# Kernel optimization log

Hardware: AMD Instinct MI355X
Metric: run time of the kernel (lower is better)

## Reference

```python
import jax, jax.numpy as jnp
import numpy as np


def setup_inputs() -> dict:
    key = jax.random.key(0)
    k1, k2, k3 = jax.random.split(key, 3)
    CAP, IN_F, OUT_F = 262144, 512, 512
    query = jax.random.normal(k1, (IN_F,), dtype=jnp.float32)
    keys = jax.random.normal(k2, (CAP, IN_F), dtype=jnp.float32)
    values = jax.random.normal(k3, (CAP, OUT_F), dtype=jnp.float32)
    return {"query": query, "keys": keys, "values": values}


def reference(query, keys, values):
    # L1 distance of query to every key: [capacity]
    attention = -jnp.sum(jnp.abs(keys - query), axis=1)
    # softmax over the capacity dimension
    attention = jax.nn.softmax(attention, axis=0)
    # attention-weighted sum of values: [out_features]
    out = jnp.matmul(attention, values)
    out = jax.nn.sigmoid(out)
    return out
```

## Files before the change

### kernel.cpp

```cpp
#include <hip/hip_runtime.h>
#include <math.h>

typedef float f32x4 __attribute__((ext_vector_type(4)));

constexpr int CAP = 262144;
constexpr int NF  = 512;

constexpr int G1  = 2048;
constexpr int RPB = CAP / G1;
constexpr int GR  = 64;
constexpr int RPR = G1 / GR;

constexpr float CUT = 25.0f;

__global__ __launch_bounds__(256) void k_logits(
    const float* __restrict__ q, const float* __restrict__ keys,
    float* __restrict__ logits, float* __restrict__ pm, float* __restrict__ ps)
{
    const int tid  = threadIdx.x;
    const int lane = tid & 63;
    const int wv   = tid >> 6;
    const int w    = blockIdx.x * 4 + wv;
    const int row0 = w * 32;

    const f32x4 q0 = *reinterpret_cast<const f32x4*>(q + lane * 8);
    const f32x4 q1 = *reinterpret_cast<const f32x4*>(q + lane * 8 + 4);

    float m = -INFINITY, s = 0.f;

    for (int b = 0; b < 4; ++b) {
        const int rb = row0 + b * 8;

        float d[8];
        #pragma unroll
        for (int i = 0; i < 8; ++i) {
            const float* kp = keys + (size_t)(rb + i) * NF + lane * 8;
            const f32x4 k0 = __builtin_nontemporal_load(reinterpret_cast<const f32x4*>(kp));
            const f32x4 k1 = __builtin_nontemporal_load(reinterpret_cast<const f32x4*>(kp + 4));
            d[i] = fabsf(k0[0] - q0[0]) + fabsf(k0[1] - q0[1])
                 + fabsf(k0[2] - q0[2]) + fabsf(k0[3] - q0[3])
                 + fabsf(k1[0] - q1[0]) + fabsf(k1[1] - q1[1])
                 + fabsf(k1[2] - q1[2]) + fabsf(k1[3] - q1[3]);
        }

        float p[4];
        #pragma unroll
        for (int i = 0; i < 4; ++i) {
            const float x = d[2 * i], y = d[2 * i + 1];
            const float keep = (lane & 1) ? y : x;
            const float send = (lane & 1) ? x : y;
            p[i] = keep + __shfl_xor(send, 1, 64);
        }
        float e[2];
        #pragma unroll
        for (int i = 0; i < 2; ++i) {
            const float x = p[2 * i], y = p[2 * i + 1];
            const float keep = (lane & 2) ? y : x;
            const float send = (lane & 2) ? x : y;
            e[i] = keep + __shfl_xor(send, 2, 64);
        }
        {
            const float keep = (lane & 4) ? e[1] : e[0];
            const float send = (lane & 4) ? e[0] : e[1];
            e[0] = keep + __shfl_xor(send, 4, 64);
        }
        float r = e[0];
        r += __shfl_xor(r, 8, 64);
        r += __shfl_xor(r, 16, 64);
        r += __shfl_xor(r, 32, 64);

        const float L = -r;
        if (lane < 8) logits[rb + lane] = L;

        const float Mn = fmaxf(m, L);
        s = s * __expf(m - Mn) + __expf(L - Mn);
        m = Mn;
    }

    s *= 0.125f;
    #pragma unroll
    for (int off = 1; off < 64; off <<= 1) {
        const float m2 = __shfl_xor(m, off, 64);
        const float s2 = __shfl_xor(s, off, 64);
        const float Mn = fmaxf(m, m2);
        s = s * __expf(m - Mn) + s2 * __expf(m2 - Mn);
        m = Mn;
    }

    __shared__ float sm[4], ss[4];
    if (lane == 0) { sm[wv] = m; ss[wv] = s; }
    __syncthreads();
    if (tid == 0) {
        float M = sm[0], S = ss[0];
        #pragma unroll
        for (int i = 1; i < 4; ++i) {
            const float Mn = fmaxf(M, sm[i]);
            S = S * __expf(M - Mn) + ss[i] * __expf(sm[i] - Mn);
            M = Mn;
        }
        pm[blockIdx.x] = M;
        ps[blockIdx.x] = S;
    }
}

__global__ __launch_bounds__(256) void k_combine(
    const float* __restrict__ pm, const float* __restrict__ ps,
    float* __restrict__ scal)
{
    const int tid = threadIdx.x;
    float M = -INFINITY, S = 0.f;
    for (int i = tid; i < G1; i += 256) {
        const float m2 = pm[i], s2 = ps[i];
        const float Mn = fmaxf(M, m2);
        S = S * __expf(M - Mn) + s2 * __expf(m2 - Mn);
        M = Mn;
    }
    #pragma unroll
    for (int off = 1; off < 64; off <<= 1) {
        const float m2 = __shfl_xor(M, off, 64);
        const float s2 = __shfl_xor(S, off, 64);
        const float Mn = fmaxf(M, m2);
        S = S * __expf(M - Mn) + s2 * __expf(m2 - Mn);
        M = Mn;
    }
    __shared__ float sm[4], ss[4];
    const int lane = tid & 63, wv = tid >> 6;
    if (lane == 0) { sm[wv] = M; ss[wv] = S; }
    __syncthreads();
    if (tid == 0) {
        float Mg = sm[0], Sg = ss[0];
        #pragma unroll
        for (int i = 1; i < 4; ++i) {
            const float Mn = fmaxf(Mg, sm[i]);
            Sg = Sg * __expf(Mg - Mn) + ss[i] * __expf(sm[i] - Mn);
            Mg = Mn;
        }
        scal[0] = Mg;
        scal[1] = 1.f / Sg;
    }
}

__global__ __launch_bounds__(256) void k_wsum_sparse(
    const float* __restrict__ vals, const float* __restrict__ logits,
    const float* __restrict__ pm, const float* __restrict__ scal,
    float* __restrict__ partial)
{
    const float M  = scal[0];
    const float mb = pm[blockIdx.x];
    if (mb < M - CUT) return;

    const int tid = threadIdx.x;
    const int col = (tid & 127) * 4;
    const int rg  = tid >> 7;
    const size_t gr0 = (size_t)blockIdx.x * RPB;

    f32x4 acc = {0.f, 0.f, 0.f, 0.f};
    for (int r = rg; r < RPB; r += 2) {
        const float L = logits[gr0 + r];
        if (L < M - CUT) continue;
        const float w = __expf(L - mb);
        const f32x4 v = *reinterpret_cast<const f32x4*>(vals + (gr0 + r) * NF + col);
        acc += w * v;
    }

    __shared__ float sp[NF];
    if (rg == 0) *reinterpret_cast<f32x4*>(sp + col) = acc;
    __syncthreads();
    if (rg == 1) {
        sp[col + 0] += acc[0]; sp[col + 1] += acc[1];
        sp[col + 2] += acc[2]; sp[col + 3] += acc[3];
    }
    __syncthreads();
    if (rg == 0)
        *reinterpret_cast<f32x4*>(partial + (size_t)blockIdx.x * NF + col) =
            *reinterpret_cast<const f32x4*>(sp + col);
}

__global__ __launch_bounds__(256) void k_red(
    const float* __restrict__ pm, const float* __restrict__ scal,
    const float* __restrict__ partial, float* __restrict__ part2)
{
    const float M = scal[0];
    const int tid = threadIdx.x;
    const int col = (tid & 127) * 4;
    const int rg  = tid >> 7;
    const int r0  = blockIdx.x * RPR;

    f32x4 acc = {0.f, 0.f, 0.f, 0.f};
    for (int r = r0 + rg; r < r0 + RPR; r += 2) {
        const float mbr = pm[r];
        if (mbr < M - CUT) continue;
        const float sc = __expf(mbr - M);
        const f32x4 v = *reinterpret_cast<const f32x4*>(partial + (size_t)r * NF + col);
        acc += sc * v;
    }

    __shared__ float sp[NF];
    if (rg == 0) *reinterpret_cast<f32x4*>(sp + col) = acc;
    __syncthreads();
    if (rg == 1) {
        sp[col + 0] += acc[0]; sp[col + 1] += acc[1];
        sp[col + 2] += acc[2]; sp[col + 3] += acc[3];
    }
    __syncthreads();
    if (rg == 0)
        *reinterpret_cast<f32x4*>(part2 + (size_t)blockIdx.x * NF + col) =
            *reinterpret_cast<const f32x4*>(sp + col);
}

__global__ __launch_bounds__(256) void k_final(
    const float* __restrict__ pm, const float* __restrict__ ps,
    const float* __restrict__ part2, float* __restrict__ out)
{
    const int tid  = threadIdx.x;
    const int lane = tid & 63;
    const int wv   = tid >> 6;

    float mx = -INFINITY;
    for (int i = tid; i < G1; i += 256) mx = fmaxf(mx, pm[i]);
    #pragma unroll
    for (int off = 1; off < 64; off <<= 1) mx = fmaxf(mx, __shfl_xor(mx, off, 64));
    __shared__ float sm[4], ss[4];
    if (lane == 0) sm[wv] = mx;
    __syncthreads();
    const float M = fmaxf(fmaxf(sm[0], sm[1]), fmaxf(sm[2], sm[3]));

    float sacc = 0.f;
    for (int i = tid; i < G1; i += 256) sacc += ps[i] * __expf(pm[i] - M);
    #pragma unroll
    for (int off = 1; off < 64; off <<= 1) sacc += __shfl_xor(sacc, off, 64);
    if (lane == 0) ss[wv] = sacc;
    __syncthreads();
    const float invS = 1.f / (ss[0] + ss[1] + ss[2] + ss[3]);

    const int o = blockIdx.x * 256 + tid;
    float acc = 0.f;
    #pragma unroll 8
    for (int j = 0; j < GR; ++j) acc += part2[(size_t)j * NF + o];
    out[o] = 1.f / (1.f + __expf(-acc * invS));
}

extern "C" void kernel_launch(void* const* d_in, const int* in_sizes, int n_in,
                              void* d_out, int out_size, void* d_ws, size_t ws_size,
                              hipStream_t stream)
{
    const float* q    = (const float*)d_in[0];
    const float* keys = (const float*)d_in[1];
    const float* vals = (const float*)d_in[2];
    float* out = (float*)d_out;

    float* ws      = (float*)d_ws;
    float* logits  = ws;
    float* pm      = logits + CAP;
    float* ps      = pm + G1;
    float* scal    = ps + G1;
    float* partial = scal + 4;
    float* part2   = partial + (size_t)G1 * NF;

    k_logits     <<<G1, 256, 0, stream>>>(q, keys, logits, pm, ps);
    k_combine    <<<1,  256, 0, stream>>>(pm, ps, scal);
    k_wsum_sparse<<<G1, 256, 0, stream>>>(vals, logits, pm, scal, partial);
    k_red        <<<GR, 256, 0, stream>>>(pm, scal, partial, part2);
    k_final      <<<2,  256, 0, stream>>>(pm, ps, part2, out);
}
```

Measured before the change: 125.1 us.

## Prefetch key rows into registers and fold global-max combine into consumers

In the logits kernel, the next 8 key rows are loaded into registers before the current batch's distances are reduced, so loads overlap with arithmetic. The separate single-block combine kernel is removed; the weighted-sum, reduction and final kernels each recompute the global max from the per-block maxima. This saves a kernel launch and a serial dependency. In exchange, every block rereads the 2048 block maxima and register pressure rises in the logits kernel.

After: 117.6 us (median of 3 runs). 6.0% less time.

```diff
diff --git a/kernel.cpp b/kernel.cpp
--- a/kernel.cpp
+++ b/kernel.cpp
@@ -13,6 +13,26 @@
 
 constexpr float CUT = 25.0f;
 
+__device__ __forceinline__ void load8(const float* __restrict__ keys, int rb,
+                                      int lane, f32x4* K0, f32x4* K1)
+{
+    #pragma unroll
+    for (int i = 0; i < 8; ++i) {
+        const float* kp = keys + (size_t)(rb + i) * NF + lane * 8;
+        K0[i] = __builtin_nontemporal_load(reinterpret_cast<const f32x4*>(kp));
+        K1[i] = __builtin_nontemporal_load(reinterpret_cast<const f32x4*>(kp + 4));
+    }
+}
+
+__device__ __forceinline__ float dist2(const f32x4 k0, const f32x4 k1,
+                                       const f32x4 q0, const f32x4 q1)
+{
+    return fabsf(k0[0] - q0[0]) + fabsf(k0[1] - q0[1])
+         + fabsf(k0[2] - q0[2]) + fabsf(k0[3] - q0[3])
+         + fabsf(k1[0] - q1[0]) + fabsf(k1[1] - q1[1])
+         + fabsf(k1[2] - q1[2]) + fabsf(k1[3] - q1[3]);
+}
+
 __global__ __launch_bounds__(256) void k_logits(
     const float* __restrict__ q, const float* __restrict__ keys,
     float* __restrict__ logits, float* __restrict__ pm, float* __restrict__ ps)
@@ -28,20 +48,18 @@
 
     float m = -INFINITY, s = 0.f;
 
+    f32x4 K0[8], K1[8];
+    load8(keys, row0, lane, K0, K1);
+
+    #pragma unroll
     for (int b = 0; b < 4; ++b) {
         const int rb = row0 + b * 8;
 
         float d[8];
         #pragma unroll
-        for (int i = 0; i < 8; ++i) {
-            const float* kp = keys + (size_t)(rb + i) * NF + lane * 8;
-            const f32x4 k0 = __builtin_nontemporal_load(reinterpret_cast<const f32x4*>(kp));
-            const f32x4 k1 = __builtin_nontemporal_load(reinterpret_cast<const f32x4*>(kp + 4));
-            d[i] = fabsf(k0[0] - q0[0]) + fabsf(k0[1] - q0[1])
-                 + fabsf(k0[2] - q0[2]) + fabsf(k0[3] - q0[3])
-                 + fabsf(k1[0] - q1[0]) + fabsf(k1[1] - q1[1])
-                 + fabsf(k1[2] - q1[2]) + fabsf(k1[3] - q1[3]);
-        }
+        for (int i = 0; i < 8; ++i) d[i] = dist2(K0[i], K1[i], q0, q1);
+
+        if (b < 3) load8(keys, rb + 8, lane, K0, K1);
 
         float p[4];
         #pragma unroll
@@ -103,53 +121,31 @@
     }
 }
 
-__global__ __launch_bounds__(256) void k_combine(
-    const float* __restrict__ pm, const float* __restrict__ ps,
-    float* __restrict__ scal)
-{
-    const int tid = threadIdx.x;
-    float M = -INFINITY, S = 0.f;
-    for (int i = tid; i < G1; i += 256) {
-        const float m2 = pm[i], s2 = ps[i];
-        const float Mn = fmaxf(M, m2);
-        S = S * __expf(M - Mn) + s2 * __expf(m2 - Mn);
-        M = Mn;
-    }
-    #pragma unroll
-    for (int off = 1; off < 64; off <<= 1) {
-        const float m2 = __shfl_xor(M, off, 64);
-        const float s2 = __shfl_xor(S, off, 64);
-        const float Mn = fmaxf(M, m2);
-        S = S * __expf(M - Mn) + s2 * __expf(m2 - Mn);
-        M = Mn;
-    }
-    __shared__ float sm[4], ss[4];
-    const int lane = tid & 63, wv = tid >> 6;
-    if (lane == 0) { sm[wv] = M; ss[wv] = S; }
-    __syncthreads();
-    if (tid == 0) {
-        float Mg = sm[0], Sg = ss[0];
-        #pragma unroll
-        for (int i = 1; i < 4; ++i) {
-            const float Mn = fmaxf(Mg, sm[i]);
-            Sg = Sg * __expf(Mg - Mn) + ss[i] * __expf(sm[i] - Mn);
-            Mg = Mn;
-        }
-        scal[0] = Mg;
-        scal[1] = 1.f / Sg;
-    }
+__device__ __forceinline__ float global_max(const float* __restrict__ pm,
+                                            int tid, int lane, int wv)
+{
+    float mx = -INFINITY;
+    for (int i = tid; i < G1; i += 256) mx = fmaxf(mx, pm[i]);
+    #pragma unroll
+    for (int off = 1; off < 64; off <<= 1) mx = fmaxf(mx, __shfl_xor(mx, off, 64));
+    __shared__ float smx[4];
+    if (lane == 0) smx[wv] = mx;
+    __syncthreads();
+    return fmaxf(fmaxf(smx[0], smx[1]), fmaxf(smx[2], smx[3]));
 }
 
 __global__ __launch_bounds__(256) void k_wsum_sparse(
     const float* __restrict__ vals, const float* __restrict__ logits,
-    const float* __restrict__ pm, const float* __restrict__ scal,
-    float* __restrict__ partial)
-{
-    const float M  = scal[0];
+    const float* __restrict__ pm, float* __restrict__ partial)
+{
+    const int tid  = threadIdx.x;
+    const int lane = tid & 63;
+    const int wv   = tid >> 6;
+
+    const float M  = global_max(pm, tid, lane, wv);
     const float mb = pm[blockIdx.x];
     if (mb < M - CUT) return;
 
-    const int tid = threadIdx.x;
     const int col = (tid & 127) * 4;
     const int rg  = tid >> 7;
     const size_t gr0 = (size_t)blockIdx.x * RPB;
@@ -177,11 +173,15 @@
 }
 
 __global__ __launch_bounds__(256) void k_red(
-    const float* __restrict__ pm, const float* __restrict__ scal,
-    const float* __restrict__ partial, float* __restrict__ part2)
-{
-    const float M = scal[0];
-    const int tid = threadIdx.x;
+    const float* __restrict__ pm, const float* __restrict__ partial,
+    float* __restrict__ part2)
+{
+    const int tid  = threadIdx.x;
+    const int lane = tid & 63;
+    const int wv   = tid >> 6;
+
+    const float M = global_max(pm, tid, lane, wv);
+
     const int col = (tid & 127) * 4;
     const int rg  = tid >> 7;
     const int r0  = blockIdx.x * RPR;
@@ -216,19 +216,13 @@
     const int lane = tid & 63;
     const int wv   = tid >> 6;
 
-    float mx = -INFINITY;
-    for (int i = tid; i < G1; i += 256) mx = fmaxf(mx, pm[i]);
-    #pragma unroll
-    for (int off = 1; off < 64; off <<= 1) mx = fmaxf(mx, __shfl_xor(mx, off, 64));
-    __shared__ float sm[4], ss[4];
-    if (lane == 0) sm[wv] = mx;
-    __syncthreads();
-    const float M = fmaxf(fmaxf(sm[0], sm[1]), fmaxf(sm[2], sm[3]));
+    const float M = global_max(pm, tid, lane, wv);
 
     float sacc = 0.f;
     for (int i = tid; i < G1; i += 256) sacc += ps[i] * __expf(pm[i] - M);
     #pragma unroll
     for (int off = 1; off < 64; off <<= 1) sacc += __shfl_xor(sacc, off, 64);
+    __shared__ float ss[4];
     if (lane == 0) ss[wv] = sacc;
     __syncthreads();
     const float invS = 1.f / (ss[0] + ss[1] + ss[2] + ss[3]);
@@ -253,13 +247,11 @@
     float* logits  = ws;
     float* pm      = logits + CAP;
     float* ps      = pm + G1;
-    float* scal    = ps + G1;
-    float* partial = scal + 4;
+    float* partial = ps + G1;
     float* part2   = partial + (size_t)G1 * NF;
 
     k_logits     <<<G1, 256, 0, stream>>>(q, keys, logits, pm, ps);
-    k_combine    <<<1,  256, 0, stream>>>(pm, ps, scal);
-    k_wsum_sparse<<<G1, 256, 0, stream>>>(vals, logits, pm, scal, partial);
-    k_red        <<<GR, 256, 0, stream>>>(pm, scal, partial, part2);
+    k_wsum_sparse<<<G1, 256, 0, stream>>>(vals, logits, pm, partial);
+    k_red        <<<GR, 256, 0, stream>>>(pm, partial, part2);
     k_final      <<<2,  256, 0, stream>>>(pm, ps, part2, out);
 }
```
